# Optimization experiments

Hardware: AMD Instinct MI355X
Metric: run time of the kernel (lower is better)

## Reference

```python
import jax, jax.numpy as jnp
import numpy as np

BETA = 0.9
THR = 1.0
ALPHA = 2.0  # snntorch ATan surrogate default

@jax.custom_vjp
def spike(x):
    # Heaviside spike with ATan surrogate gradient (snntorch default)
    return (x > 0).astype(x.dtype)

def _spike_fwd(x):
    return spike(x), x

def _spike_bwd(x, g):
    grad = (ALPHA / 2.0) / (1.0 + (jnp.pi / 2.0 * ALPHA * x) ** 2)
    return (g * grad,)

spike.defvjp(_spike_fwd, _spike_bwd)

def setup_inputs() -> dict:
    key = jax.random.key(0)
    k1, k2, k3 = jax.random.split(key, 3)
    T, B, NI, NH, NO = 250, 256, 700, 1024, 20
    input_spikes = (jax.random.uniform(k1, (T, B, NI)) < 0.1).astype(jnp.float32)
    W1 = jax.random.normal(k2, (NH, NI), dtype=jnp.float32) / np.float32(np.sqrt(NI))
    W2 = jax.random.normal(k3, (NO, NH), dtype=jnp.float32) / np.float32(np.sqrt(NH))
    return {"input_spikes": input_spikes, "W1": W1, "W2": W2}

def reference(input_spikes, W1, W2):
    # fc1 over all timesteps in one GEMM: [T,B,NI] x [NH,NI] -> [T,B,NH]
    cur1 = jnp.einsum('tbi,hi->tbh', input_spikes, W1)

    # snntorch Leaky (reset_mechanism='subtract'):
    #   reset = detach(heaviside(mem_prev - thr))
    #   mem   = beta*mem_prev + cur - reset*thr
    #   spk   = heaviside(mem - thr)
    def lif_step(mem, c):
        reset = jax.lax.stop_gradient(spike(mem - THR))
        mem = BETA * mem + c - reset * THR
        spk = spike(mem - THR)
        return mem, spk

    mem0 = jnp.zeros(cur1.shape[1:], cur1.dtype)
    _, spk1 = jax.lax.scan(lif_step, mem0, cur1)  # [T,B,NH]

    # fc2 over all timesteps: [T,B,NH] x [NO,NH] -> [T,B,NO]
    cur2 = jnp.einsum('tbh,oh->tbo', spk1, W2)

    # Readout: Leaky with reset_mechanism='none' -> mem = beta*mem + cur
    def ro_step(mem, c):
        mem = BETA * mem + c
        return mem, mem

    m0 = jnp.zeros(cur2.shape[1:], cur2.dtype)
    _, mem_out_rec = jax.lax.scan(ro_step, m0, cur2)  # [T,B,NO]

    out_rec = jax.nn.softmax(mem_out_rec, axis=2)  # torch softmax dim=1 on [B,NO]
    return mem_out_rec, out_rec
```

## Files before the change

### kernel.cpp

```cpp
#include <hip/hip_runtime.h>
#include <hip/hip_bf16.h>
#include <cstdint>

#define T_STEPS 250
#define BATCH   256
#define NI      700
#define NH      1024
#define NO      20
#define BETAF   0.9f
#define KPAD    704
#define KT_N    22
#define KCAT    2112

typedef __attribute__((ext_vector_type(8))) short bf16x8;
typedef __attribute__((ext_vector_type(4))) float f32x4;

static __device__ __forceinline__ unsigned short f2bu(float x) {
    union { __hip_bfloat16 h; unsigned short u; } c;
    c.h = __float2bfloat16(x);
    return c.u;
}
static __device__ __forceinline__ float b2f(unsigned short u) {
    union { __hip_bfloat16 h; unsigned short u; } c;
    c.u = u;
    return __bfloat162float(c.h);
}

__global__ __launch_bounds__(256) void k0_init(const float* __restrict__ W1,
                                               const float* __restrict__ W2,
                                               float* __restrict__ W2T,
                                               float* __restrict__ mem1,
                                               unsigned short* __restrict__ Bcat) {
    int idx = blockIdx.x * 256 + threadIdx.x;
    if (idx < BATCH * NH) mem1[idx] = 0.f;
    if (idx < NH * NO) {
        int h = idx / NO, o = idx % NO;
        W2T[idx] = W2[o * NH + h];
    }
    if (idx < NH * KPAD) {
        int n = idx / KPAD, k = idx % KPAD;
        float w = (k < NI) ? W1[n * NI + k] : 0.f;
        unsigned short hu = f2bu(w);
        float r1 = w - b2f(hu);
        unsigned short mu = f2bu(r1);
        float r2 = r1 - b2f(mu);
        unsigned short lu = f2bu(r2);
        unsigned short* row = Bcat + (size_t)n * KCAT + k;
        row[0]        = hu;
        row[KPAD]     = mu;
        row[2 * KPAD] = lu;
    }
}

__global__ __launch_bounds__(256) void k1_cvt(const float* __restrict__ A,
                                              unsigned short* __restrict__ Abf,
                                              int rows) {
    int idx = blockIdx.x * 256 + threadIdx.x;
    int r = idx / 176, q = idx - r * 176;
    if (r >= rows) return;
    int k = q * 4;
    ushort4 o = make_ushort4(0, 0, 0, 0);
    if (k < NI) {
        float4 v = *(const float4*)(A + (size_t)r * NI + k);
        o.x = f2bu(v.x); o.y = f2bu(v.y); o.z = f2bu(v.z); o.w = f2bu(v.w);
    }
    *(ushort4*)(Abf + (size_t)r * KPAD + k) = o;
}

__global__ __launch_bounds__(256) void k2_fc1(const unsigned short* __restrict__ Abf,
                                              const unsigned short* __restrict__ Bcat,
                                              float* __restrict__ C) {
    __shared__ unsigned short As[128 * 32];
    __shared__ unsigned short Bs[3][128 * 32];
    const int tid  = threadIdx.x;
    const int lane = tid & 63;
    const int wv   = tid >> 6;

    int nwg = gridDim.x, bid = blockIdx.x, w;
    if ((nwg & 7) == 0) w = (bid & 7) * (nwg >> 3) + (bid >> 3);
    else                w = bid;
    const int brow = (w >> 3) * 128;
    const int bn   = (w & 7) * 128;
    const int wm   = (wv >> 1) * 64;
    const int wn   = (wv & 1) * 64;

    f32x4 acc[4][4];
#pragma unroll
    for (int i = 0; i < 4; ++i)
#pragma unroll
        for (int j = 0; j < 4; ++j) acc[i][j] = (f32x4){0.f, 0.f, 0.f, 0.f};

    auto stage = [&](const unsigned short* gbase, int rstride, int kcol,
                     unsigned short* lds) {
#pragma unroll
        for (int j = 0; j < 2; ++j) {
            int c   = wv * 128 + j * 64 + lane;
            int row = c >> 2;
            int lk  = ((c & 3) ^ ((row >> 1) & 3)) * 8;
            const unsigned short* src = gbase + (size_t)row * rstride + kcol + lk;
            __builtin_amdgcn_global_load_lds(
                (const __attribute__((address_space(1))) void*)src,
                (__attribute__((address_space(3))) void*)(lds + (wv * 128 + j * 64) * 8),
                16, 0, 0);
        }
    };

    const unsigned short* Ab = Abf + (size_t)brow * KPAD;
    const unsigned short* Bb = Bcat + (size_t)bn * KCAT;

    const int frow = lane & 15;
    const int fsl  = (((lane >> 4) & 3) ^ ((frow >> 1) & 3)) * 8;

    for (int kt = 0; kt < KT_N; ++kt) {
        stage(Ab, KPAD, kt * 32, As);
#pragma unroll
        for (int s = 0; s < 3; ++s)
            stage(Bb, KCAT, s * KPAD + kt * 32, Bs[s]);
        __syncthreads();

        bf16x8 a[4];
#pragma unroll
        for (int i = 0; i < 4; ++i)
            a[i] = *(const bf16x8*)&As[(wm + i * 16 + frow) * 32 + fsl];
#pragma unroll
        for (int s = 0; s < 3; ++s) {
#pragma unroll
            for (int j = 0; j < 4; ++j) {
                bf16x8 b = *(const bf16x8*)&Bs[s][(wn + j * 16 + frow) * 32 + fsl];
#pragma unroll
                for (int i = 0; i < 4; ++i)
                    acc[i][j] = __builtin_amdgcn_mfma_f32_16x16x32_bf16(a[i], b, acc[i][j], 0, 0, 0);
            }
        }
        __syncthreads();
    }

#pragma unroll
    for (int i = 0; i < 4; ++i) {
#pragma unroll
        for (int j = 0; j < 4; ++j) {
            int col  = bn + wn + j * 16 + (lane & 15);
            int row0 = brow + wm + i * 16 + ((lane >> 4) << 2);
#pragma unroll
            for (int q = 0; q < 4; ++q)
                C[(size_t)(row0 + q) * NH + col] = acc[i][j][q];
        }
    }
}

__global__ __launch_bounds__(256) void k3_lif(const float* __restrict__ cur1,
                                              float* __restrict__ mem1,
                                              unsigned long long* __restrict__ bits,
                                              int TC) {
    int b = blockIdx.x >> 2;
    int hg = blockIdx.x & 3;
    int h = hg * 256 + threadIdx.x;
    const size_t S = (size_t)BATCH * NH;
    const float* p = cur1 + (size_t)b * NH + h;
    unsigned long long* bp = bits + (size_t)b * 16 + hg * 4 + (threadIdx.x >> 6);
    const bool lead = (threadIdx.x & 63) == 0;
    float mem = mem1[b * NH + h];

#define LIF_STEP(cv, t)                                                        \
    {                                                                          \
        float reset = (mem > 1.0f) ? 1.0f : 0.0f;                              \
        mem = fmaf(BETAF, mem, (cv)) - reset;                                  \
        unsigned long long mk = __ballot(mem > 1.0f);                          \
        if (lead) bp[(size_t)(t) * (BATCH * 16)] = mk;                         \
    }

    float c0 = (0 < TC) ? p[0] : 0.f;
    float c1 = (1 < TC) ? p[S] : 0.f;
    float c2 = (2 < TC) ? p[2 * S] : 0.f;
    float c3 = (3 < TC) ? p[3 * S] : 0.f;
    int tc = 0;
    for (; tc + 4 <= TC; tc += 4) {
        LIF_STEP(c0, tc + 0); if (tc + 4 < TC) c0 = p[(size_t)(tc + 4) * S];
        LIF_STEP(c1, tc + 1); if (tc + 5 < TC) c1 = p[(size_t)(tc + 5) * S];
        LIF_STEP(c2, tc + 2); if (tc + 6 < TC) c2 = p[(size_t)(tc + 6) * S];
        LIF_STEP(c3, tc + 3); if (tc + 7 < TC) c3 = p[(size_t)(tc + 7) * S];
    }
    for (; tc < TC; ++tc) { float c = p[(size_t)tc * S]; LIF_STEP(c, tc); }
#undef LIF_STEP
    mem1[b * NH + h] = mem;
}

__global__ __launch_bounds__(256) void k4_fc2(const unsigned long long* __restrict__ bits,
                                              const float* __restrict__ W2T,
                                              float* __restrict__ cur2) {
    int row = blockIdx.x * 4 + (threadIdx.x >> 6);
    int lane = threadIdx.x & 63;
    unsigned long long mv = (lane < 16) ? bits[(size_t)row * 16 + lane] : 0ULL;
    float p = 0.f;
#pragma unroll 1
    for (int wseg = 0; wseg < 16; ++wseg) {
        unsigned long long m = __shfl(mv, wseg);
        while (m) {
            int bit = __ffsll((unsigned long long)m) - 1;
            m &= m - 1;
            int h = wseg * 64 + bit;
            if (lane < NO) p += W2T[h * NO + lane];
        }
    }
    if (lane < NO) cur2[(size_t)row * NO + lane] = p;
}

__global__ __launch_bounds__(256) void k5_readout(const float* __restrict__ cur2,
                                                  float* __restrict__ out_mem,
                                                  float* __restrict__ out_sm) {
    int b = blockIdx.x * 8 + (threadIdx.x >> 5);
    int o = threadIdx.x & 31;
    bool act = o < NO;
    const float* p = cur2 + (size_t)b * NO + (act ? o : 0);
    float mem = 0.f;
    float nxt = p[0];
    for (int t = 0; t < T_STEPS; ++t) {
        float c = nxt;
        if (t + 1 < T_STEPS) nxt = p[(size_t)(t + 1) * BATCH * NO];
        mem = fmaf(BETAF, mem, c);
        float e = act ? __expf(mem) : 0.f;
        float s = e;
#pragma unroll
        for (int off = 16; off; off >>= 1) s += __shfl_xor(s, off, 32);
        if (act) {
            int base = (t * BATCH + b) * NO;
            out_mem[base + o] = mem;
            out_sm[base + o] = __fdividef(e, s);
        }
    }
}

extern "C" void kernel_launch(void* const* d_in, const int* in_sizes, int n_in,
                              void* d_out, int out_size, void* d_ws, size_t ws_size,
                              hipStream_t stream) {
    const float* spikes = (const float*)d_in[0];
    const float* W1     = (const float*)d_in[1];
    const float* W2     = (const float*)d_in[2];
    float* out_mem = (float*)d_out;
    float* out_sm  = out_mem + (size_t)T_STEPS * BATCH * NO;

    char* ws = (char*)d_ws;
    size_t off = 0;
    auto alloc = [&](size_t bytes) -> char* {
        off = (off + 255) & ~(size_t)255;
        char* p = ws + off;
        off += bytes;
        return p;
    };
    float*          W2T  = (float*)alloc((size_t)NH * NO * 4);
    float*          mem1 = (float*)alloc((size_t)BATCH * NH * 4);
    float*          cur2 = (float*)alloc((size_t)T_STEPS * BATCH * NO * 4);
    unsigned short* Bcat = (unsigned short*)alloc((size_t)NH * KCAT * 2);

    size_t fixed = (off + 255) & ~(size_t)255;
    size_t rem = ws_size > fixed ? ws_size - fixed : 0;
    size_t per_t = (size_t)BATCH * NH * 4 + (size_t)BATCH * KPAD * 2
                 + (size_t)BATCH * 16 * 8 + 768;
    int TC = (int)(rem / per_t);
    if (TC > T_STEPS) TC = T_STEPS;
    if (TC < 1) TC = 1;
    float*              cur1 = (float*)alloc((size_t)TC * BATCH * NH * 4);
    unsigned short*     Abf  = (unsigned short*)alloc((size_t)TC * BATCH * KPAD * 2);
    unsigned long long* bits = (unsigned long long*)alloc((size_t)TC * BATCH * 16 * 8);

    k0_init<<<(NH * KPAD + 255) / 256, 256, 0, stream>>>(W1, W2, W2T, mem1, Bcat);

    for (int t0 = 0; t0 < T_STEPS; t0 += TC) {
        int tc = T_STEPS - t0 < TC ? T_STEPS - t0 : TC;
        int rows = tc * BATCH;
        k1_cvt<<<(rows * 176 + 255) / 256, 256, 0, stream>>>(
            spikes + (size_t)t0 * BATCH * NI, Abf, rows);
        int nwg = (rows / 128) * 8;
        k2_fc1<<<nwg, 256, 0, stream>>>(Abf, Bcat, cur1);
        k3_lif<<<1024, 256, 0, stream>>>(cur1, mem1, bits, tc);
        k4_fc2<<<tc * 64, 256, 0, stream>>>(bits, W2T, cur2 + (size_t)t0 * BATCH * NO);
    }

    k5_readout<<<32, 256, 0, stream>>>(cur2, out_mem, out_sm);
}
```

Before: 528.1 us.

## Fuse LIF recurrence with sparse fc2 accumulation into one per-batch kernel

Merges the LIF scan kernel and the spike-driven fc2 kernel into a single kernel with one block per batch row. Each wave handles 256 hidden units (4 per lane), ballots spikes, and immediately sums the W2 columns for the set bits; partial sums from the waves are reduced through shared memory each timestep. This drops the spike-bitmask buffer round trip and one kernel launch per chunk. In exchange, parallelism falls from 1024 to 256 blocks, each timestep needs two block barriers, and the serial ffs loops in the critical path may lengthen the recurrence.

```diff
diff --git a/kernel.cpp b/kernel.cpp
--- a/kernel.cpp
+++ b/kernel.cpp
@@ -148,61 +148,80 @@
     }
 }
 
-__global__ __launch_bounds__(256) void k3_lif(const float* __restrict__ cur1,
-                                              float* __restrict__ mem1,
-                                              unsigned long long* __restrict__ bits,
-                                              int TC) {
-    int b = blockIdx.x >> 2;
-    int hg = blockIdx.x & 3;
-    int h = hg * 256 + threadIdx.x;
+__global__ __launch_bounds__(256) void k34_lif_fc2(const float* __restrict__ cur1,
+                                                   float* __restrict__ mem1,
+                                                   const float* __restrict__ W2T,
+                                                   float* __restrict__ cur2,
+                                                   int TC, int tg0) {
+    __shared__ float part[3][NO];
+    const int b    = blockIdx.x;
+    const int wv   = threadIdx.x >> 6;
+    const int lane = threadIdx.x & 63;
+    const bool act = lane < NO;
+    const int hb   = wv * 256;
     const size_t S = (size_t)BATCH * NH;
-    const float* p = cur1 + (size_t)b * NH + h;
-    unsigned long long* bp = bits + (size_t)b * 16 + hg * 4 + (threadIdx.x >> 6);
-    const bool lead = (threadIdx.x & 63) == 0;
-    float mem = mem1[b * NH + h];
-
-#define LIF_STEP(cv, t)                                                        \
+    const float* p = cur1 + (size_t)b * NH + hb + lane;
+    float*      mp = mem1 + b * NH + hb + lane;
+    const float* W = W2T + (act ? lane : 0);
+
+    float m0 = mp[0], m1 = mp[64], m2 = mp[128], m3 = mp[192];
+
+    auto ld = [&](int t, int j) -> float {
+        int tt = t < TC ? t : TC - 1;
+        return p[(size_t)tt * S + j * 64];
+    };
+
+#define K34_STEP(c0, c1, c2, c3, T)                                            \
     {                                                                          \
-        float reset = (mem > 1.0f) ? 1.0f : 0.0f;                              \
-        mem = fmaf(BETAF, mem, (cv)) - reset;                                  \
-        unsigned long long mk = __ballot(mem > 1.0f);                          \
-        if (lead) bp[(size_t)(t) * (BATCH * 16)] = mk;                         \
-    }
-
-    float c0 = (0 < TC) ? p[0] : 0.f;
-    float c1 = (1 < TC) ? p[S] : 0.f;
-    float c2 = (2 < TC) ? p[2 * S] : 0.f;
-    float c3 = (3 < TC) ? p[3 * S] : 0.f;
-    int tc = 0;
-    for (; tc + 4 <= TC; tc += 4) {
-        LIF_STEP(c0, tc + 0); if (tc + 4 < TC) c0 = p[(size_t)(tc + 4) * S];
-        LIF_STEP(c1, tc + 1); if (tc + 5 < TC) c1 = p[(size_t)(tc + 5) * S];
-        LIF_STEP(c2, tc + 2); if (tc + 6 < TC) c2 = p[(size_t)(tc + 6) * S];
-        LIF_STEP(c3, tc + 3); if (tc + 7 < TC) c3 = p[(size_t)(tc + 7) * S];
-    }
-    for (; tc < TC; ++tc) { float c = p[(size_t)tc * S]; LIF_STEP(c, tc); }
-#undef LIF_STEP
-    mem1[b * NH + h] = mem;
-}
-
-__global__ __launch_bounds__(256) void k4_fc2(const unsigned long long* __restrict__ bits,
-                                              const float* __restrict__ W2T,
-                                              float* __restrict__ cur2) {
-    int row = blockIdx.x * 4 + (threadIdx.x >> 6);
-    int lane = threadIdx.x & 63;
-    unsigned long long mv = (lane < 16) ? bits[(size_t)row * 16 + lane] : 0ULL;
-    float p = 0.f;
-#pragma unroll 1
-    for (int wseg = 0; wseg < 16; ++wseg) {
-        unsigned long long m = __shfl(mv, wseg);
-        while (m) {
-            int bit = __ffsll((unsigned long long)m) - 1;
-            m &= m - 1;
-            int h = wseg * 64 + bit;
-            if (lane < NO) p += W2T[h * NO + lane];
-        }
-    }
-    if (lane < NO) cur2[(size_t)row * NO + lane] = p;
+        float r0 = m0 > 1.f ? 1.f : 0.f;                                       \
+        m0 = fmaf(BETAF, m0, (c0)) - r0;                                       \
+        unsigned long long w0 = __ballot(m0 > 1.f);                            \
+        float r1 = m1 > 1.f ? 1.f : 0.f;                                       \
+        m1 = fmaf(BETAF, m1, (c1)) - r1;                                       \
+        unsigned long long w1 = __ballot(m1 > 1.f);                            \
+        float r2 = m2 > 1.f ? 1.f : 0.f;                                       \
+        m2 = fmaf(BETAF, m2, (c2)) - r2;                                       \
+        unsigned long long w2 = __ballot(m2 > 1.f);                            \
+        float r3 = m3 > 1.f ? 1.f : 0.f;                                       \
+        m3 = fmaf(BETAF, m3, (c3)) - r3;                                       \
+        unsigned long long w3 = __ballot(m3 > 1.f);                            \
+        float g0 = 0.f, g1 = 0.f;                                              \
+        { unsigned long long m = w0;                                           \
+          while (m) { int bt = __ffsll(m) - 1; m &= m - 1;                     \
+                      g0 += W[(hb + bt) * NO]; } }                             \
+        { unsigned long long m = w1;                                           \
+          while (m) { int bt = __ffsll(m) - 1; m &= m - 1;                     \
+                      g1 += W[(hb + 64 + bt) * NO]; } }                        \
+        { unsigned long long m = w2;                                           \
+          while (m) { int bt = __ffsll(m) - 1; m &= m - 1;                     \
+                      g0 += W[(hb + 128 + bt) * NO]; } }                       \
+        { unsigned long long m = w3;                                           \
+          while (m) { int bt = __ffsll(m) - 1; m &= m - 1;                     \
+                      g1 += W[(hb + 192 + bt) * NO]; } }                       \
+        float g = g0 + g1;                                                     \
+        if (wv != 0 && act) part[wv - 1][lane] = g;                            \
+        __syncthreads();                                                       \
+        if (wv == 0 && act)                                                    \
+            cur2[((size_t)(tg0 + (T)) * BATCH + b) * NO + lane] =              \
+                g + part[0][lane] + part[1][lane] + part[2][lane];             \
+        __syncthreads();                                                       \
+    }
+
+    float a0 = ld(0, 0), a1 = ld(0, 1), a2 = ld(0, 2), a3 = ld(0, 3);
+    float e0 = ld(1, 0), e1 = ld(1, 1), e2 = ld(1, 2), e3 = ld(1, 3);
+
+    for (int t = 0; t < TC; t += 2) {
+        K34_STEP(a0, a1, a2, a3, t);
+        a0 = ld(t + 2, 0); a1 = ld(t + 2, 1);
+        a2 = ld(t + 2, 2); a3 = ld(t + 2, 3);
+        if (t + 1 < TC) {
+            K34_STEP(e0, e1, e2, e3, t + 1);
+            e0 = ld(t + 3, 0); e1 = ld(t + 3, 1);
+            e2 = ld(t + 3, 2); e3 = ld(t + 3, 3);
+        }
+    }
+#undef K34_STEP
+    mp[0] = m0; mp[64] = m1; mp[128] = m2; mp[192] = m3;
 }
 
 __global__ __launch_bounds__(256) void k5_readout(const float* __restrict__ cur2,
@@ -254,14 +273,12 @@
 
     size_t fixed = (off + 255) & ~(size_t)255;
     size_t rem = ws_size > fixed ? ws_size - fixed : 0;
-    size_t per_t = (size_t)BATCH * NH * 4 + (size_t)BATCH * KPAD * 2
-                 + (size_t)BATCH * 16 * 8 + 768;
+    size_t per_t = (size_t)BATCH * NH * 4 + (size_t)BATCH * KPAD * 2 + 768;
     int TC = (int)(rem / per_t);
     if (TC > T_STEPS) TC = T_STEPS;
     if (TC < 1) TC = 1;
-    float*              cur1 = (float*)alloc((size_t)TC * BATCH * NH * 4);
-    unsigned short*     Abf  = (unsigned short*)alloc((size_t)TC * BATCH * KPAD * 2);
-    unsigned long long* bits = (unsigned long long*)alloc((size_t)TC * BATCH * 16 * 8);
+    float*          cur1 = (float*)alloc((size_t)TC * BATCH * NH * 4);
+    unsigned short* Abf  = (unsigned short*)alloc((size_t)TC * BATCH * KPAD * 2);
 
     k0_init<<<(NH * KPAD + 255) / 256, 256, 0, stream>>>(W1, W2, W2T, mem1, Bcat);
 
@@ -272,8 +289,7 @@
             spikes + (size_t)t0 * BATCH * NI, Abf, rows);
         int nwg = (rows / 128) * 8;
         k2_fc1<<<nwg, 256, 0, stream>>>(Abf, Bcat, cur1);
-        k3_lif<<<1024, 256, 0, stream>>>(cur1, mem1, bits, tc);
-        k4_fc2<<<tc * 64, 256, 0, stream>>>(bits, W2T, cur2 + (size_t)t0 * BATCH * NO);
+        k34_lif_fc2<<<BATCH, 256, 0, stream>>>(cur1, mem1, W2T, cur2, tc, t0);
     }
 
     k5_readout<<<32, 256, 0, stream>>>(cur2, out_mem, out_sm);
```

New measurement: 858.7 us. +62.6%, slower.

## Split fc2 spike-sparse gather across four wavefronts per row with dual accumulators

Applied to the files above, without the earlier changes.

The fc2 kernel now assigns one workgroup per (t,b) row instead of one wavefront per row. Each of the four wavefronts handles 256 hidden units and reduces its partial sums through shared memory. The bit-scan loop is also unrolled to pop two set bits per iteration into two independent accumulators, which raises memory-level parallelism on the W2T gathers. In exchange it launches four times as many workgroups and adds a block barrier plus a shared-memory reduction per row.

```diff
diff --git a/kernel.cpp b/kernel.cpp
--- a/kernel.cpp
+++ b/kernel.cpp
@@ -188,21 +188,35 @@
 __global__ __launch_bounds__(256) void k4_fc2(const unsigned long long* __restrict__ bits,
                                               const float* __restrict__ W2T,
                                               float* __restrict__ cur2) {
-    int row = blockIdx.x * 4 + (threadIdx.x >> 6);
+    __shared__ float part[4][NO];
+    int row  = blockIdx.x;
+    int wv   = threadIdx.x >> 6;
     int lane = threadIdx.x & 63;
-    unsigned long long mv = (lane < 16) ? bits[(size_t)row * 16 + lane] : 0ULL;
-    float p = 0.f;
-#pragma unroll 1
-    for (int wseg = 0; wseg < 16; ++wseg) {
-        unsigned long long m = __shfl(mv, wseg);
+    bool act = lane < NO;
+    unsigned long long mv = (lane < 4) ? bits[(size_t)row * 16 + wv * 4 + lane] : 0ULL;
+    const float* W = W2T + (act ? lane : 0);
+    float p0 = 0.f, p1 = 0.f;
+#pragma unroll
+    for (int i = 0; i < 4; ++i) {
+        unsigned long long m = __shfl(mv, i);
+        int base = (wv * 4 + i) * 64;
         while (m) {
-            int bit = __ffsll((unsigned long long)m) - 1;
-            m &= m - 1;
-            int h = wseg * 64 + bit;
-            if (lane < NO) p += W2T[h * NO + lane];
-        }
-    }
-    if (lane < NO) cur2[(size_t)row * NO + lane] = p;
+            int  b0 = __ffsll(m) - 1;            m &= m - 1;
+            bool v1 = m != 0;
+            int  b1 = v1 ? __ffsll(m) - 1 : 0;   m &= m - 1;
+            float w0 = W[(base + b0) * NO];
+            float w1 = W[(base + b1) * NO];
+            p0 += w0;
+            p1 += v1 ? w1 : 0.f;
+        }
+    }
+    float p = p0 + p1;
+    if (wv != 0 && act) part[wv][lane] = p;
+    __syncthreads();
+    if (wv == 0 && act) {
+        p += part[1][lane] + part[2][lane] + part[3][lane];
+        cur2[(size_t)row * NO + lane] = p;
+    }
 }
 
 __global__ __launch_bounds__(256) void k5_readout(const float* __restrict__ cur2,
@@ -273,7 +287,7 @@
         int nwg = (rows / 128) * 8;
         k2_fc1<<<nwg, 256, 0, stream>>>(Abf, Bcat, cur1);
         k3_lif<<<1024, 256, 0, stream>>>(cur1, mem1, bits, tc);
-        k4_fc2<<<tc * 64, 256, 0, stream>>>(bits, W2T, cur2 + (size_t)t0 * BATCH * NO);
+        k4_fc2<<<rows, 256, 0, stream>>>(bits, W2T, cur2 + (size_t)t0 * BATCH * NO);
     }
 
     k5_readout<<<32, 256, 0, stream>>>(cur2, out_mem, out_sm);
```

After: 533.3 us. About the same (+1.0%).
